# Kernel tuning notes

Hardware: AMD Instinct MI355X
Metric: run time of the kernel (lower is better)

The kernel has to match this reference:

```python
import jax, jax.numpy as jnp
import numpy as np

SKIP = 91
PREEMPH = 0.85
N = 33554432  # 2**25 samples


def setup_inputs() -> dict:
    key = jax.random.key(0)
    sig = jax.random.normal(key, (N,), dtype=jnp.float32) * 0.1
    return {"sig": sig}


def _preemph_scan(y, coef):
    # First-order IIR: out[0] = y[0]; out[i] = y[i] + coef * out[i-1]
    # Expressed as an associative scan over pairs (a, b) representing x -> a*x + b.
    a = jnp.full_like(y, coef)

    def combine(e1, e2):
        a1, b1 = e1
        a2, b2 = e2
        return a1 * a2, b2 + a2 * b1

    _, out = jax.lax.associative_scan(combine, (a, y))
    return out


def reference(sig):
    y = _preemph_scan(sig, jnp.float32(PREEMPH))
    # drop first `skip` samples, zero-pad the tail (same length)
    y = jnp.concatenate([y[SKIP:], jnp.zeros((SKIP,), dtype=y.dtype)])
    out = jnp.clip(32768.0 * y, -32768.0, 32767.0).astype(jnp.int16)
    return out
```

## Files before the change

### kernel.cpp

```cpp
#include <hip/hip_runtime.h>


#define BLOCK   256
#define CH      16
#define TILE    (BLOCK * CH)
#define SKIP    91
#define WARM    71
#define COEF    0.85f
#define NREAD   88
#define PAD4(p) ((p) + 4 * ((p) >> 5))
#define LDS_F   4608

typedef int v4i __attribute__((ext_vector_type(4)));

__global__ __launch_bounds__(BLOCK, 8) void preemph_kernel(
        const float* __restrict__ sig, int* __restrict__ out, int n) {
    __shared__ float lds[LDS_F];
    const int  tid      = threadIdx.x;
    const long tileBase = (long)blockIdx.x * TILE;
    const long tStart   = tileBase + (SKIP - WARM);
    const long g0       = tStart + (long)tid * CH;

    float acc = 0.f;
    int   res[CH];

    const bool safe = (tStart + (long)(BLOCK - 1) * CH + NREAD) <= (long)n;

    if (safe) {
        const float4* __restrict__ p = reinterpret_cast<const float4*>(sig + g0);
#pragma unroll
        for (int k = 0; k < NREAD / 4; ++k) {
            float4 v = p[k];
#pragma unroll
            for (int c = 0; c < 4; ++c) {
                const int e = 4 * k + c;
                float x = (c == 0) ? v.x : (c == 1) ? v.y : (c == 2) ? v.z : v.w;
                if (e < WARM) {
                    acc = fmaf(acc, COEF, x);
                } else if (e < WARM + CH) {
                    acc = fmaf(acc, COEF, x);
                    float s = acc * 32768.f;
                    s = fminf(fmaxf(s, -32768.f), 32767.f);
                    res[e - WARM] = (int)s;
                }
            }
        }
    } else {
#pragma unroll
        for (int e = 0; e < WARM + CH; ++e) {
            long g = g0 + e;
            float x = (g < (long)n) ? sig[g] : 0.f;
            acc = fmaf(acc, COEF, x);
            if (e >= WARM) {
                float s = acc * 32768.f;
                s = fminf(fmaxf(s, -32768.f), 32767.f);
                res[e - WARM] = (int)s;
            }
        }
    }

    const long oBase = tileBase + (long)tid * CH;
    const long oLim  = (long)n - SKIP;
#pragma unroll
    for (int j = 0; j < CH; ++j)
        if (oBase + j >= oLim) res[j] = 0;

    float4* const l4 = reinterpret_cast<float4*>(lds);
    const int p0 = tid * CH;
#pragma unroll
    for (int k = 0; k < 4; ++k) {
        float4 v;
        v.x = __int_as_float(res[4 * k + 0]);
        v.y = __int_as_float(res[4 * k + 1]);
        v.z = __int_as_float(res[4 * k + 2]);
        v.w = __int_as_float(res[4 * k + 3]);
        l4[PAD4(p0 + 4 * k) >> 2] = v;
    }
    __syncthreads();

#pragma unroll
    for (int k = 0; k < 4; ++k) {
        int  off = k * (BLOCK * 4) + tid * 4;
        long o   = tileBase + off;
        float4 v = l4[PAD4(off) >> 2];
        v4i iv;
        iv.x = __float_as_int(v.x);
        iv.y = __float_as_int(v.y);
        iv.z = __float_as_int(v.z);
        iv.w = __float_as_int(v.w);
        if (o + 3 < (long)n) {
            __builtin_nontemporal_store(iv, reinterpret_cast<v4i*>(out + o));
        } else {
            if (o + 0 < (long)n) out[o + 0] = iv.x;
            if (o + 1 < (long)n) out[o + 1] = iv.y;
            if (o + 2 < (long)n) out[o + 2] = iv.z;
        }
    }
}

extern "C" void kernel_launch(void* const* d_in, const int* in_sizes, int n_in,
                              void* d_out, int out_size, void* d_ws, size_t ws_size,
                              hipStream_t stream) {
    const float* sig = (const float*)d_in[0];
    int* out = (int*)d_out;
    int n = in_sizes[0];
    int grid = (int)(((long)n + TILE - 1) / TILE);
    preemph_kernel<<<grid, BLOCK, 0, stream>>>(sig, out, n);
}
```

Baseline: 257.1 us.

## Replace per-thread warm-up recurrence with wave-level shuffle scan over chunks

Drops the per-thread approach, where each thread redoes 71 warm-up samples before its 16 outputs. Each wave now scans a 4096-sample segment in chunks of 256 using a shuffle-based parallel prefix with precomputed coefficient powers. Each chunk's carry passes to the next, and a single warm-up chunk seeds the first. This removes the redundant warm-up reads and FMAs and the LDS transpose, and prefetches the next chunk. In exchange it adds shuffle latency, a serial carry chain across chunks, and a changed grid mapping.

```diff
diff --git a/kernel.cpp b/kernel.cpp
--- a/kernel.cpp
+++ b/kernel.cpp
@@ -2,99 +2,121 @@
 
 
 #define BLOCK   256
-#define CH      16
-#define TILE    (BLOCK * CH)
 #define SKIP    91
-#define WARM    71
 #define COEF    0.85f
-#define NREAD   88
-#define PAD4(p) ((p) + 4 * ((p) >> 5))
-#define LDS_F   4608
+#define CHUNK_N 256
+#define CHUNKS  16
+#define SEG     (CHUNKS * CHUNK_N)
+#define WPB     (BLOCK / 64)
+#define TILE    (WPB * SEG)
 
 typedef int v4i __attribute__((ext_vector_type(4)));
 
+__device__ __forceinline__ int cvt16(float v) {
+    float s = v * 32768.f;
+    s = fminf(fmaxf(s, -32768.f), 32767.f);
+    return (int)s;
+}
+
+__device__ __forceinline__ float4 ld_chunk(const float* __restrict__ sig,
+                                           long yb, long n, bool safe) {
+    if (safe) return *reinterpret_cast<const float4*>(sig + yb);
+    float4 x;
+    x.x = (yb + 0 >= 0 && yb + 0 < n) ? sig[yb + 0] : 0.f;
+    x.y = (yb + 1 >= 0 && yb + 1 < n) ? sig[yb + 1] : 0.f;
+    x.z = (yb + 2 >= 0 && yb + 2 < n) ? sig[yb + 2] : 0.f;
+    x.w = (yb + 3 >= 0 && yb + 3 < n) ? sig[yb + 3] : 0.f;
+    return x;
+}
+
 __global__ __launch_bounds__(BLOCK, 8) void preemph_kernel(
         const float* __restrict__ sig, int* __restrict__ out, int n) {
-    __shared__ float lds[LDS_F];
-    const int  tid      = threadIdx.x;
-    const long tileBase = (long)blockIdx.x * TILE;
-    const long tStart   = tileBase + (SKIP - WARM);
-    const long g0       = tStart + (long)tid * CH;
+    const long ln   = n;
+    const int  lane = threadIdx.x & 63;
+    const long segBase = (long)blockIdx.x * TILE + (long)(threadIdx.x >> 6) * SEG;
+    if (segBase >= ln) return;
 
-    float acc = 0.f;
-    int   res[CH];
+    const float K1  = COEF * COEF * COEF * COEF;
+    const float K2  = K1 * K1;
+    const float K4  = K2 * K2;
+    const float K8  = K4 * K4;
+    const float K16 = K8 * K8;
+    const float C1 = COEF, C2 = COEF * COEF, C3 = C2 * COEF, C4 = K1;
+    const float wpow = exp2f((float)(lane + 1) * (4.0f * -0.23446525109f));
 
-    const bool safe = (tStart + (long)(BLOCK - 1) * CH + NREAD) <= (long)n;
+    float s0, s1, s2, s3;
+    auto wscan = [&](const float4& x) -> float {
+        s0 = x.x;
+        s1 = fmaf(s0, COEF, x.y);
+        s2 = fmaf(s1, COEF, x.z);
+        s3 = fmaf(s2, COEF, x.w);
+        float t = s3, u;
+        u = __shfl_up(t, 1, 64);  t = (lane >= 1)  ? fmaf(u, K1,  t) : t;
+        u = __shfl_up(t, 2, 64);  t = (lane >= 2)  ? fmaf(u, K2,  t) : t;
+        u = __shfl_up(t, 4, 64);  t = (lane >= 4)  ? fmaf(u, K4,  t) : t;
+        u = __shfl_up(t, 8, 64);  t = (lane >= 8)  ? fmaf(u, K8,  t) : t;
+        u = __shfl_up(t, 16, 64); t = (lane >= 16) ? fmaf(u, K16, t) : t;
+        return t;
+    };
 
-    if (safe) {
-        const float4* __restrict__ p = reinterpret_cast<const float4*>(sig + g0);
-#pragma unroll
-        for (int k = 0; k < NREAD / 4; ++k) {
-            float4 v = p[k];
-#pragma unroll
-            for (int c = 0; c < 4; ++c) {
-                const int e = 4 * k + c;
-                float x = (c == 0) ? v.x : (c == 1) ? v.y : (c == 2) ? v.z : v.w;
-                if (e < WARM) {
-                    acc = fmaf(acc, COEF, x);
-                } else if (e < WARM + CH) {
-                    acc = fmaf(acc, COEF, x);
-                    float s = acc * 32768.f;
-                    s = fminf(fmaxf(s, -32768.f), 32767.f);
-                    res[e - WARM] = (int)s;
-                }
-            }
+    const bool warmSafe = (segBase >= 164);
+    float4 xw = ld_chunk(sig, segBase - 164 + 4 * (long)lane, ln, warmSafe);
+
+    bool  csafe0 = (segBase + (SKIP + 1) + CHUNK_N) <= ln;
+    float4 xc = ld_chunk(sig, segBase + (SKIP + 1) + 4 * (long)lane, ln, csafe0);
+
+    float tw   = wscan(xw);
+    float y_in = __shfl(tw, 63, 64);
+
+    const long oLim = ln - SKIP;
+
+#pragma unroll 4
+    for (int c = 0; c < CHUNKS; ++c) {
+        const long o0 = segBase + (long)c * CHUNK_N;
+        if (o0 >= ln) break;
+
+        float4 xn;
+        if (c + 1 < CHUNKS) {
+            long yn    = segBase + (SKIP + 1) + (long)(c + 1) * CHUNK_N;
+            bool snext = (yn + CHUNK_N) <= ln;
+            xn = ld_chunk(sig, yn + 4 * (long)lane, ln, snext);
         }
-    } else {
-#pragma unroll
-        for (int e = 0; e < WARM + CH; ++e) {
-            long g = g0 + e;
-            float x = (g < (long)n) ? sig[g] : 0.f;
-            acc = fmaf(acc, COEF, x);
-            if (e >= WARM) {
-                float s = acc * 32768.f;
-                s = fminf(fmaxf(s, -32768.f), 32767.f);
-                res[e - WARM] = (int)s;
-            }
+
+        float t = wscan(xc);
+        float L = fmaf(wpow, y_in, t);
+        float p = __shfl_up(L, 1, 64);
+        if (lane == 0) p = y_in;
+
+        float o0f = fmaf(p, C1, s0);
+        float o1f = fmaf(p, C2, s1);
+        float o2f = fmaf(p, C3, s2);
+        float o3f = fmaf(p, C4, s3);
+        int i0 = cvt16(o0f), i1 = cvt16(o1f), i2 = cvt16(o2f);
+        int i3 = cvt16(o3f);
+
+        int prv = __shfl_up(i3, 1, 64);
+        if (lane == 0) prv = cvt16(y_in);
+        v4i iv;
+        iv.x = prv; iv.y = i0; iv.z = i1; iv.w = i2;
+
+        y_in = __shfl(L, 63, 64);
+
+        const long ob = o0 + 4 * (long)lane;
+        if (o0 + CHUNK_N > oLim) {
+            if (ob + 0 >= oLim) iv.x = 0;
+            if (ob + 1 >= oLim) iv.y = 0;
+            if (ob + 2 >= oLim) iv.z = 0;
+            if (ob + 3 >= oLim) iv.w = 0;
         }
-    }
-
-    const long oBase = tileBase + (long)tid * CH;
-    const long oLim  = (long)n - SKIP;
-#pragma unroll
-    for (int j = 0; j < CH; ++j)
-        if (oBase + j >= oLim) res[j] = 0;
-
-    float4* const l4 = reinterpret_cast<float4*>(lds);
-    const int p0 = tid * CH;
-#pragma unroll
-    for (int k = 0; k < 4; ++k) {
-        float4 v;
-        v.x = __int_as_float(res[4 * k + 0]);
-        v.y = __int_as_float(res[4 * k + 1]);
-        v.z = __int_as_float(res[4 * k + 2]);
-        v.w = __int_as_float(res[4 * k + 3]);
-        l4[PAD4(p0 + 4 * k) >> 2] = v;
-    }
-    __syncthreads();
-
-#pragma unroll
-    for (int k = 0; k < 4; ++k) {
-        int  off = k * (BLOCK * 4) + tid * 4;
-        long o   = tileBase + off;
-        float4 v = l4[PAD4(off) >> 2];
-        v4i iv;
-        iv.x = __float_as_int(v.x);
-        iv.y = __float_as_int(v.y);
-        iv.z = __float_as_int(v.z);
-        iv.w = __float_as_int(v.w);
-        if (o + 3 < (long)n) {
-            __builtin_nontemporal_store(iv, reinterpret_cast<v4i*>(out + o));
+        if (o0 + CHUNK_N <= ln) {
+            __builtin_nontemporal_store(iv, reinterpret_cast<v4i*>(out + ob));
         } else {
-            if (o + 0 < (long)n) out[o + 0] = iv.x;
-            if (o + 1 < (long)n) out[o + 1] = iv.y;
-            if (o + 2 < (long)n) out[o + 2] = iv.z;
+            if (ob + 0 < ln) out[ob + 0] = iv.x;
+            if (ob + 1 < ln) out[ob + 1] = iv.y;
+            if (ob + 2 < ln) out[ob + 2] = iv.z;
+            if (ob + 3 < ln) out[ob + 3] = iv.w;
         }
+        xc = xn;
     }
 }
 
```

Result: faster. 235.5 us (-8.4%).
